# Kernel optimization log

Hardware: AMD Instinct MI355X
Metric: run time of the kernel (lower is better)

## Reference

```python
import jax, jax.numpy as jnp
import numpy as np

NUM_GRAPHS = 4096  # fixed number of segments for scatter_mean


def setup_inputs() -> dict:
    key = jax.random.key(0)
    ks = jax.random.split(key, 8)
    N, D, G = 1_000_000, 256, 256
    s = 1.0 / np.sqrt(D)
    x = jax.random.normal(ks[0], (N, D), dtype=jnp.float32)
    batch = jnp.sort(jax.random.randint(ks[1], (N,), 0, NUM_GRAPHS, dtype=jnp.int64))
    W = jax.random.normal(ks[2], (D, G), dtype=jnp.float32) * s
    b = jax.random.normal(ks[3], (G,), dtype=jnp.float32) * s
    Wg = jax.random.normal(ks[4], (D, G), dtype=jnp.float32) * s
    bg = jax.random.normal(ks[5], (G,), dtype=jnp.float32) * s
    Wf = jax.random.normal(ks[6], (G, G), dtype=jnp.float32) * (1.0 / np.sqrt(G))
    bf = jax.random.normal(ks[7], (G,), dtype=jnp.float32) * (1.0 / np.sqrt(G))
    return {"x": x, "batch": batch, "W": W, "b": b, "Wg": Wg, "bg": bg, "Wf": Wf, "bf": bf}


def reference(x, batch, W, b, Wg, bg, Wf, bf):
    # gated linear: states * softmax(gates) over feature dim (dim=1)
    states = x @ W + b                                   # [N, G]
    gates = jax.nn.softmax(x @ Wg + bg, axis=1)          # [N, G]
    gated = states * gates                               # [N, G]
    # scatter_mean over graph ids
    seg_sum = jax.ops.segment_sum(gated, batch, num_segments=NUM_GRAPHS)
    counts = jax.ops.segment_sum(jnp.ones((x.shape[0],), dtype=gated.dtype), batch,
                                 num_segments=NUM_GRAPHS)
    mean = seg_sum / jnp.maximum(counts, 1.0)[:, None]   # [NUM_GRAPHS, G]
    return mean @ Wf + bf
```

## Files before the change

kernel.cpp:

```cpp
#include <hip/hip_runtime.h>
#include <hip/hip_bf16.h>

typedef __attribute__((ext_vector_type(8))) short short8;
typedef __attribute__((ext_vector_type(4))) float f32x4;

#define D_DIM 256
#define G_DIM 256
#define NSEG 4096
#define BM 64

__device__ __forceinline__ unsigned f2bf_u(float f) {
  unsigned u = __builtin_bit_cast(unsigned, f);
  return (u + 0x7fffu + ((u >> 16) & 1u)) >> 16;
}
__device__ __forceinline__ unsigned pk_bf2(float a, float b) {
  __hip_bfloat162 h = __float22bfloat162_rn(float2{a, b});
  unsigned r;
  __builtin_memcpy(&r, &h, 4);
  return r;
}

__global__ void wconv_kernel(const float* __restrict__ W, const float* __restrict__ Wg,
                             unsigned short* __restrict__ Wc) {
  int j = blockIdx.x;
  int k = threadIdx.x;
  float v = (j < 256) ? W[k * 256 + j] : Wg[k * 256 + (j - 256)];
  Wc[j * 256 + k] = (unsigned short)f2bf_u(v);
}

__global__ void count_kernel(const int* __restrict__ batch, int N, float* __restrict__ counts) {
  int g = blockIdx.x * blockDim.x + threadIdx.x;
  if (g >= NSEG) return;
  int lo = 0, hi = N;
  while (lo < hi) { int mid = (lo + hi) >> 1; if (batch[mid] < g) lo = mid + 1; else hi = mid; }
  int lo2 = lo, hi2 = N;
  while (lo2 < hi2) { int mid = (lo2 + hi2) >> 1; if (batch[mid] < g + 1) lo2 = mid + 1; else hi2 = mid; }
  counts[g] = (float)(lo2 - lo);
}

__global__ __launch_bounds__(512, 4) void fused_main(
    const float* __restrict__ x, const int* __restrict__ batch,
    const unsigned short* __restrict__ Wc,
    const float* __restrict__ bvec, const float* __restrict__ bgvec,
    float* __restrict__ seg, int N) {
  __shared__ __align__(16) char xs[32768];
  __shared__ __align__(16) float part[8][64];
  __shared__ __align__(16) float sinv[64];

  const int t = threadIdx.x;
  const int lane = t & 63;
  const int wid = t >> 6;
  const int lr = lane & 15;
  const int lk = lane >> 4;
  const long row0 = (long)blockIdx.x * BM;

#pragma unroll
  for (int it = 0; it < 4; ++it) {
    int rl = it * 16 + (t >> 5);
    int kb = (t & 31) * 8;
    const float4* p = (const float4*)(x + (row0 + rl) * D_DIM + kb);
    float4 v0 = p[0], v1 = p[1];
    uint4 pk;
    pk.x = pk_bf2(v0.x, v0.y);
    pk.y = pk_bf2(v0.z, v0.w);
    pk.z = pk_bf2(v1.x, v1.y);
    pk.w = pk_bf2(v1.z, v1.w);
    int byte = (rl * 512 + kb * 2) ^ ((rl & 7) << 4);
    *(uint4*)(xs + byte) = pk;
  }
  __syncthreads();

  f32x4 acc[4][4];
#pragma unroll
  for (int m = 0; m < 4; ++m)
#pragma unroll
    for (int n = 0; n < 4; ++n) acc[m][n] = (f32x4){0.f, 0.f, 0.f, 0.f};

  const int cb = wid * 32;
#pragma unroll
  for (int kk = 0; kk < 8; ++kk) {
    const int k0 = kk * 32 + lk * 8;
    short8 a[4], bb[4];
#pragma unroll
    for (int n = 0; n < 4; ++n) {
      int col = (n < 2) ? (cb + n * 16 + lr) : (256 + cb + (n - 2) * 16 + lr);
      bb[n] = *(const short8*)(Wc + col * 256 + k0);
    }
#pragma unroll
    for (int m = 0; m < 4; ++m) {
      int row = m * 16 + lr;
      int byte = (row * 512 + k0 * 2) ^ ((row & 7) << 4);
      a[m] = *(const short8*)(xs + byte);
    }
#pragma unroll
    for (int m = 0; m < 4; ++m)
#pragma unroll
      for (int n = 0; n < 4; ++n)
        acc[m][n] = __builtin_amdgcn_mfma_f32_16x16x32_bf16(a[m], bb[n], acc[m][n], 0, 0, 0);
  }

  float bgv[2];
#pragma unroll
  for (int n = 0; n < 2; ++n) bgv[n] = bgvec[cb + n * 16 + lr];
#pragma unroll
  for (int m = 0; m < 4; ++m)
#pragma unroll
    for (int n = 2; n < 4; ++n)
#pragma unroll
      for (int q = 0; q < 4; ++q)
        acc[m][n][q] = __expf(acc[m][n][q] + bgv[n - 2]);

#pragma unroll
  for (int m = 0; m < 4; ++m) {
    float s[4];
#pragma unroll
    for (int q = 0; q < 4; ++q) {
      float v = acc[m][2][q] + acc[m][3][q];
      v += __shfl_xor(v, 1);
      v += __shfl_xor(v, 2);
      v += __shfl_xor(v, 4);
      v += __shfl_xor(v, 8);
      s[q] = v;
    }
    if (lr == 0) {
#pragma unroll
      for (int q = 0; q < 4; ++q) part[wid][m * 16 + lk * 4 + q] = s[q];
    }
  }
  __syncthreads();
  if (wid == 0) {
    float v = part[0][lane] + part[1][lane] + part[2][lane] + part[3][lane] +
              part[4][lane] + part[5][lane] + part[6][lane] + part[7][lane];
    sinv[lane] = 1.0f / v;
  }
  __syncthreads();

  float bv[2];
#pragma unroll
  for (int n = 0; n < 2; ++n) bv[n] = bvec[cb + n * 16 + lr];
  f32x4 siv[4];
#pragma unroll
  for (int m = 0; m < 4; ++m) siv[m] = *(const f32x4*)(&sinv[m * 16 + lk * 4]);
#pragma unroll
  for (int m = 0; m < 4; ++m)
#pragma unroll
    for (int n = 0; n < 2; ++n)
#pragma unroll
      for (int q = 0; q < 4; ++q)
        acc[m][n][q] = (acc[m][n][q] + bv[n]) * acc[m][n + 2][q] * siv[m][q];

  int rb[4][4];
#pragma unroll
  for (int m = 0; m < 4; ++m) {
    const int4 v = *(const int4*)(batch + row0 + m * 16 + lk * 4);
    rb[m][0] = v.x; rb[m][1] = v.y; rb[m][2] = v.z; rb[m][3] = v.w;
  }
  const int g0 = batch[row0];
  const int g1 = batch[row0 + BM - 1];
  for (int g = g0; g <= g1; ++g) {
    float p[2] = {0.f, 0.f};
#pragma unroll
    for (int m = 0; m < 4; ++m)
#pragma unroll
      for (int q = 0; q < 4; ++q) {
        bool hit = (rb[m][q] == g);
#pragma unroll
        for (int n = 0; n < 2; ++n) p[n] += hit ? acc[m][n][q] : 0.f;
      }
#pragma unroll
    for (int n = 0; n < 2; ++n) {
      p[n] += __shfl_xor(p[n], 16);
      p[n] += __shfl_xor(p[n], 32);
    }
    if (lane < 16) {
#pragma unroll
      for (int n = 0; n < 2; ++n)
        atomicAdd(seg + (long)g * G_DIM + cb + n * 16 + lane, p[n]);
    }
  }
}

__global__ __launch_bounds__(256) void final_kernel(
    float* __restrict__ seg, const float* __restrict__ counts,
    const float* __restrict__ Wf, const float* __restrict__ bfv) {
  __shared__ float mlds[16][257];
  int g0 = blockIdx.x * 16;
  int t = threadIdx.x;
#pragma unroll
  for (int i = 0; i < 16; ++i) {
    float inv = 1.0f / fmaxf(counts[g0 + i], 1.0f);
    mlds[i][t] = seg[(g0 + i) * 256 + t] * inv;
  }
  __syncthreads();
  float a[16];
#pragma unroll
  for (int i = 0; i < 16; ++i) a[i] = 0.f;
  for (int k = 0; k < 256; ++k) {
    float w = Wf[k * 256 + t];
#pragma unroll
    for (int i = 0; i < 16; ++i) a[i] += mlds[i][k] * w;
  }
  float bfx = bfv[t];
#pragma unroll
  for (int i = 0; i < 16; ++i) seg[(g0 + i) * 256 + t] = a[i] + bfx;
}

extern "C" void kernel_launch(void* const* d_in, const int* in_sizes, int n_in,
                              void* d_out, int out_size, void* d_ws, size_t ws_size,
                              hipStream_t stream) {
  const float* x = (const float*)d_in[0];
  const int* batch = (const int*)d_in[1];
  const float* W = (const float*)d_in[2];
  const float* b = (const float*)d_in[3];
  const float* Wg = (const float*)d_in[4];
  const float* bg = (const float*)d_in[5];
  const float* Wf = (const float*)d_in[6];
  const float* bf = (const float*)d_in[7];
  const int N = in_sizes[0] / D_DIM;

  unsigned short* Wc = (unsigned short*)d_ws;
  float* counts = (float*)((char*)d_ws + 262144);
  float* seg = (float*)d_out;

  (void)hipMemsetAsync(d_out, 0, (size_t)out_size * sizeof(float), stream);
  hipLaunchKernelGGL(wconv_kernel, dim3(512), dim3(256), 0, stream, W, Wg, Wc);
  hipLaunchKernelGGL(count_kernel, dim3(NSEG / 256), dim3(256), 0, stream, batch, N, counts);
  hipLaunchKernelGGL(fused_main, dim3(N / BM), dim3(512), 0, stream, x, batch, Wc, b, bg, seg, N);
  hipLaunchKernelGGL(final_kernel, dim3(NSEG / 16), dim3(256), 0, stream, seg, counts, Wf, bf);
}
```

Before: 651.4 us.

## Make fused GEMM kernel persistent with double-buffered LDS and register prefetch

The main kernel becomes persistent: 256 blocks of 1024 threads loop over the 64-row tiles, and each of the 16 waves now owns 16 output columns. The next tile's x rows are prefetched into registers while the current tile is computed, LDS is double-buffered, and B-fragment loads from global memory are software-pipelined two k-steps ahead. The aim is to hide HBM latency for x and cut per-block launch overhead. In exchange, a 1024-thread block carries heavier __syncthreads cost, and 256 blocks may not fill every CU of the device.

After: 935.3 us. +43.6%, slower.

```diff
diff --git a/kernel.cpp b/kernel.cpp
--- a/kernel.cpp
+++ b/kernel.cpp
@@ -8,6 +8,7 @@
 #define G_DIM 256
 #define NSEG 4096
 #define BM 64
+#define PBLK 256
 
 __device__ __forceinline__ unsigned f2bf_u(float f) {
   unsigned u = __builtin_bit_cast(unsigned, f);
@@ -38,13 +39,13 @@
   counts[g] = (float)(lo2 - lo);
 }
 
-__global__ __launch_bounds__(512, 4) void fused_main(
+__global__ __launch_bounds__(1024, 4) void fused_main(
     const float* __restrict__ x, const int* __restrict__ batch,
     const unsigned short* __restrict__ Wc,
     const float* __restrict__ bvec, const float* __restrict__ bgvec,
     float* __restrict__ seg, int N) {
-  __shared__ __align__(16) char xs[32768];
-  __shared__ __align__(16) float part[8][64];
+  __shared__ __align__(16) char xs[2][32768];
+  __shared__ __align__(16) float part[16][64];
   __shared__ __align__(16) float sinv[64];
 
   const int t = threadIdx.x;
@@ -52,130 +53,153 @@
   const int wid = t >> 6;
   const int lr = lane & 15;
   const int lk = lane >> 4;
-  const long row0 = (long)blockIdx.x * BM;
-
-#pragma unroll
-  for (int it = 0; it < 4; ++it) {
-    int rl = it * 16 + (t >> 5);
-    int kb = (t & 31) * 8;
-    const float4* p = (const float4*)(x + (row0 + rl) * D_DIM + kb);
-    float4 v0 = p[0], v1 = p[1];
-    uint4 pk;
-    pk.x = pk_bf2(v0.x, v0.y);
-    pk.y = pk_bf2(v0.z, v0.w);
-    pk.z = pk_bf2(v1.x, v1.y);
-    pk.w = pk_bf2(v1.z, v1.w);
-    int byte = (rl * 512 + kb * 2) ^ ((rl & 7) << 4);
-    *(uint4*)(xs + byte) = pk;
-  }
-  __syncthreads();
-
-  f32x4 acc[4][4];
-#pragma unroll
-  for (int m = 0; m < 4; ++m)
-#pragma unroll
-    for (int n = 0; n < 4; ++n) acc[m][n] = (f32x4){0.f, 0.f, 0.f, 0.f};
-
-  const int cb = wid * 32;
-#pragma unroll
-  for (int kk = 0; kk < 8; ++kk) {
-    const int k0 = kk * 32 + lk * 8;
-    short8 a[4], bb[4];
-#pragma unroll
-    for (int n = 0; n < 4; ++n) {
-      int col = (n < 2) ? (cb + n * 16 + lr) : (256 + cb + (n - 2) * 16 + lr);
-      bb[n] = *(const short8*)(Wc + col * 256 + k0);
-    }
-#pragma unroll
-    for (int m = 0; m < 4; ++m) {
-      int row = m * 16 + lr;
-      int byte = (row * 512 + k0 * 2) ^ ((row & 7) << 4);
-      a[m] = *(const short8*)(xs + byte);
-    }
+  const int cb = wid * 16;
+  const int ntiles = N / BM;
+
+  const int srl = t >> 5;
+  const int skb = (t & 31) * 8;
+  const int sby0 = (srl * 512 + skb * 2) ^ ((srl & 7) << 4);
+  const int sby1 = ((srl + 32) * 512 + skb * 2) ^ (((srl + 32) & 7) << 4);
+
+  const unsigned short* Bs = Wc + (cb + lr) * 256 + lk * 8;
+  const unsigned short* Bg = Wc + (256 + cb + lr) * 256 + lk * 8;
+
+  int abase[4], asw[4];
+#pragma unroll
+  for (int m = 0; m < 4; ++m) {
+    int ar = m * 16 + lr;
+    abase[m] = ar * 512;
+    asw[m] = (ar & 7) << 4;
+  }
+  const int ko2 = lk * 16;
+
+  const float bgv = bgvec[cb + lr];
+  const float bv = bvec[cb + lr];
+
+  int tile = blockIdx.x;
+  float4 ld0, ld1, ld2, ld3;
+  {
+    const float* p0 = x + (long)(tile * BM + srl) * D_DIM + skb;
+    ld0 = ((const float4*)p0)[0];
+    ld1 = ((const float4*)p0)[1];
+    const float* p1 = p0 + 32 * D_DIM;
+    ld2 = ((const float4*)p1)[0];
+    ld3 = ((const float4*)p1)[1];
+  }
+
+  for (int it = 0; tile < ntiles; ++it, tile += PBLK) {
+    char* xb = xs[it & 1];
+    const long row0 = (long)tile * BM;
+
+    {
+      uint4 pk0, pk1;
+      pk0.x = pk_bf2(ld0.x, ld0.y); pk0.y = pk_bf2(ld0.z, ld0.w);
+      pk0.z = pk_bf2(ld1.x, ld1.y); pk0.w = pk_bf2(ld1.z, ld1.w);
+      pk1.x = pk_bf2(ld2.x, ld2.y); pk1.y = pk_bf2(ld2.z, ld2.w);
+      pk1.z = pk_bf2(ld3.x, ld3.y); pk1.w = pk_bf2(ld3.z, ld3.w);
+      *(uint4*)(xb + sby0) = pk0;
+      *(uint4*)(xb + sby1) = pk1;
+    }
+    if (tile + PBLK < ntiles) {
+      const float* p0 = x + ((long)(tile + PBLK) * BM + srl) * D_DIM + skb;
+      ld0 = ((const float4*)p0)[0];
+      ld1 = ((const float4*)p0)[1];
+      const float* p1 = p0 + 32 * D_DIM;
+      ld2 = ((const float4*)p1)[0];
+      ld3 = ((const float4*)p1)[1];
+    }
+
+    short8 bcur0 = *(const short8*)(Bs);
+    short8 bcur1 = *(const short8*)(Bg);
+    short8 bnxt0 = *(const short8*)(Bs + 32);
+    short8 bnxt1 = *(const short8*)(Bg + 32);
+
+    __syncthreads();
+
+    f32x4 acc[4][2];
+#pragma unroll
+    for (int m = 0; m < 4; ++m) {
+      acc[m][0] = (f32x4){0.f, 0.f, 0.f, 0.f};
+      acc[m][1] = (f32x4){0.f, 0.f, 0.f, 0.f};
+    }
+
+#pragma unroll
+    for (int kk = 0; kk < 8; ++kk) {
+      short8 a[4];
+#pragma unroll
+      for (int m = 0; m < 4; ++m)
+        a[m] = *(const short8*)(xb + abase[m] + ((kk * 64 + ko2) ^ asw[m]));
+      short8 b0 = bcur0, b1 = bcur1;
+      bcur0 = bnxt0; bcur1 = bnxt1;
+      if (kk < 6) {
+        bnxt0 = *(const short8*)(Bs + (kk + 2) * 32);
+        bnxt1 = *(const short8*)(Bg + (kk + 2) * 32);
+      }
+#pragma unroll
+      for (int m = 0; m < 4; ++m) {
+        acc[m][0] = __builtin_amdgcn_mfma_f32_16x16x32_bf16(a[m], b0, acc[m][0], 0, 0, 0);
+        acc[m][1] = __builtin_amdgcn_mfma_f32_16x16x32_bf16(a[m], b1, acc[m][1], 0, 0, 0);
+      }
+    }
+
 #pragma unroll
     for (int m = 0; m < 4; ++m)
 #pragma unroll
-      for (int n = 0; n < 4; ++n)
-        acc[m][n] = __builtin_amdgcn_mfma_f32_16x16x32_bf16(a[m], bb[n], acc[m][n], 0, 0, 0);
-  }
-
-  float bgv[2];
-#pragma unroll
-  for (int n = 0; n < 2; ++n) bgv[n] = bgvec[cb + n * 16 + lr];
-#pragma unroll
-  for (int m = 0; m < 4; ++m)
-#pragma unroll
-    for (int n = 2; n < 4; ++n)
-#pragma unroll
       for (int q = 0; q < 4; ++q)
-        acc[m][n][q] = __expf(acc[m][n][q] + bgv[n - 2]);
-
-#pragma unroll
-  for (int m = 0; m < 4; ++m) {
-    float s[4];
-#pragma unroll
-    for (int q = 0; q < 4; ++q) {
-      float v = acc[m][2][q] + acc[m][3][q];
-      v += __shfl_xor(v, 1);
-      v += __shfl_xor(v, 2);
-      v += __shfl_xor(v, 4);
-      v += __shfl_xor(v, 8);
-      s[q] = v;
-    }
-    if (lr == 0) {
-#pragma unroll
-      for (int q = 0; q < 4; ++q) part[wid][m * 16 + lk * 4 + q] = s[q];
-    }
-  }
-  __syncthreads();
-  if (wid == 0) {
-    float v = part[0][lane] + part[1][lane] + part[2][lane] + part[3][lane] +
-              part[4][lane] + part[5][lane] + part[6][lane] + part[7][lane];
-    sinv[lane] = 1.0f / v;
-  }
-  __syncthreads();
-
-  float bv[2];
-#pragma unroll
-  for (int n = 0; n < 2; ++n) bv[n] = bvec[cb + n * 16 + lr];
-  f32x4 siv[4];
-#pragma unroll
-  for (int m = 0; m < 4; ++m) siv[m] = *(const f32x4*)(&sinv[m * 16 + lk * 4]);
-#pragma unroll
-  for (int m = 0; m < 4; ++m)
-#pragma unroll
-    for (int n = 0; n < 2; ++n)
+        acc[m][1][q] = __expf(acc[m][1][q] + bgv);
+
+#pragma unroll
+    for (int m = 0; m < 4; ++m) {
+      float s[4];
+#pragma unroll
+      for (int q = 0; q < 4; ++q) {
+        float v = acc[m][1][q];
+        v += __shfl_xor(v, 1);
+        v += __shfl_xor(v, 2);
+        v += __shfl_xor(v, 4);
+        v += __shfl_xor(v, 8);
+        s[q] = v;
+      }
+      if (lr == 0) {
+#pragma unroll
+        for (int q = 0; q < 4; ++q) part[wid][m * 16 + lk * 4 + q] = s[q];
+      }
+    }
+    __syncthreads();
+    if (wid == 0) {
+      float v = 0.f;
+#pragma unroll
+      for (int w = 0; w < 16; ++w) v += part[w][lane];
+      sinv[lane] = 1.0f / v;
+    }
+    __syncthreads();
+
+#pragma unroll
+    for (int m = 0; m < 4; ++m) {
+      f32x4 siv = *(const f32x4*)(&sinv[m * 16 + lk * 4]);
 #pragma unroll
       for (int q = 0; q < 4; ++q)
-        acc[m][n][q] = (acc[m][n][q] + bv[n]) * acc[m][n + 2][q] * siv[m][q];
-
-  int rb[4][4];
-#pragma unroll
-  for (int m = 0; m < 4; ++m) {
-    const int4 v = *(const int4*)(batch + row0 + m * 16 + lk * 4);
-    rb[m][0] = v.x; rb[m][1] = v.y; rb[m][2] = v.z; rb[m][3] = v.w;
-  }
-  const int g0 = batch[row0];
-  const int g1 = batch[row0 + BM - 1];
-  for (int g = g0; g <= g1; ++g) {
-    float p[2] = {0.f, 0.f};
-#pragma unroll
-    for (int m = 0; m < 4; ++m)
-#pragma unroll
-      for (int q = 0; q < 4; ++q) {
-        bool hit = (rb[m][q] == g);
-#pragma unroll
-        for (int n = 0; n < 2; ++n) p[n] += hit ? acc[m][n][q] : 0.f;
-      }
-#pragma unroll
-    for (int n = 0; n < 2; ++n) {
-      p[n] += __shfl_xor(p[n], 16);
-      p[n] += __shfl_xor(p[n], 32);
-    }
-    if (lane < 16) {
-#pragma unroll
-      for (int n = 0; n < 2; ++n)
-        atomicAdd(seg + (long)g * G_DIM + cb + n * 16 + lane, p[n]);
+        acc[m][0][q] = (acc[m][0][q] + bv) * acc[m][1][q] * siv[q];
+    }
+
+    int rb[4][4];
+#pragma unroll
+    for (int m = 0; m < 4; ++m) {
+      const int4 v = *(const int4*)(batch + row0 + m * 16 + lk * 4);
+      rb[m][0] = v.x; rb[m][1] = v.y; rb[m][2] = v.z; rb[m][3] = v.w;
+    }
+    const int g0 = batch[row0];
+    const int g1 = batch[row0 + BM - 1];
+    for (int g = g0; g <= g1; ++g) {
+      float p = 0.f;
+#pragma unroll
+      for (int m = 0; m < 4; ++m)
+#pragma unroll
+        for (int q = 0; q < 4; ++q)
+          p += (rb[m][q] == g) ? acc[m][0][q] : 0.f;
+      p += __shfl_xor(p, 16);
+      p += __shfl_xor(p, 32);
+      if (lane < 16) atomicAdd(seg + (long)g * G_DIM + cb + lane, p);
     }
   }
 }
@@ -225,6 +249,6 @@
   (void)hipMemsetAsync(d_out, 0, (size_t)out_size * sizeof(float), stream);
   hipLaunchKernelGGL(wconv_kernel, dim3(512), dim3(256), 0, stream, W, Wg, Wc);
   hipLaunchKernelGGL(count_kernel, dim3(NSEG / 256), dim3(256), 0, stream, batch, N, counts);
-  hipLaunchKernelGGL(fused_main, dim3(N / BM), dim3(512), 0, stream, x, batch, Wc, b, bg, seg, N);
+  hipLaunchKernelGGL(fused_main, dim3(PBLK), dim3(1024), 0, stream, x, batch, Wc, b, bg, seg, N);
   hipLaunchKernelGGL(final_kernel, dim3(NSEG / 16), dim3(256), 0, stream, seg, counts, Wf, bf);
 }
```

## Make fused kernel persistent with double-buffered x tiles and carried segment accumulation

Applied to the files above, without the earlier changes.

The fused GEMM/softmax/scatter kernel becomes persistent: 256 blocks each walk a contiguous range of 64-row tiles. The next tile's x is prefetched into registers and staged into a second LDS buffer while the current tile is computed. B-operand loads are software-pipelined across k steps. Segment partial sums are carried across tiles, so atomics are issued only when the graph id changes, which cuts atomic traffic. The cost is that only 256 blocks (occupancy hint 2) must saturate HBM bandwidth, leaving less latency hiding than many small blocks would give.

Result: slower. 861.2 us (+32.2%).

```diff
diff --git a/kernel.cpp b/kernel.cpp
--- a/kernel.cpp
+++ b/kernel.cpp
@@ -8,6 +8,7 @@
 #define G_DIM 256
 #define NSEG 4096
 #define BM 64
+#define PBLK 256
 
 __device__ __forceinline__ unsigned f2bf_u(float f) {
   unsigned u = __builtin_bit_cast(unsigned, f);
@@ -38,12 +39,12 @@
   counts[g] = (float)(lo2 - lo);
 }
 
-__global__ __launch_bounds__(512, 4) void fused_main(
+__global__ __launch_bounds__(512, 2) void fused_main(
     const float* __restrict__ x, const int* __restrict__ batch,
     const unsigned short* __restrict__ Wc,
     const float* __restrict__ bvec, const float* __restrict__ bgvec,
     float* __restrict__ seg, int N) {
-  __shared__ __align__(16) char xs[32768];
+  __shared__ __align__(16) char xs[2][32768];
   __shared__ __align__(16) float part[8][64];
   __shared__ __align__(16) float sinv[64];
 
@@ -52,132 +53,208 @@
   const int wid = t >> 6;
   const int lr = lane & 15;
   const int lk = lane >> 4;
-  const long row0 = (long)blockIdx.x * BM;
-
+  const int cb = wid * 32;
+  const int ntiles = N / BM;
+
+  const int q = ntiles / PBLK, r = ntiles % PBLK;
+  const int bid = blockIdx.x;
+  const int t0 = bid * q + (bid < r ? bid : r);
+  const int t1 = t0 + q + (bid < r ? 1 : 0);
+
+  const int srl = t >> 5;
+  const int skb = (t & 31) * 8;
+  int sby[4];
 #pragma unroll
   for (int it = 0; it < 4; ++it) {
-    int rl = it * 16 + (t >> 5);
-    int kb = (t & 31) * 8;
-    const float4* p = (const float4*)(x + (row0 + rl) * D_DIM + kb);
-    float4 v0 = p[0], v1 = p[1];
-    uint4 pk;
-    pk.x = pk_bf2(v0.x, v0.y);
-    pk.y = pk_bf2(v0.z, v0.w);
-    pk.z = pk_bf2(v1.x, v1.y);
-    pk.w = pk_bf2(v1.z, v1.w);
-    int byte = (rl * 512 + kb * 2) ^ ((rl & 7) << 4);
-    *(uint4*)(xs + byte) = pk;
-  }
+    int rl = it * 16 + srl;
+    sby[it] = (rl * 512 + skb * 2) ^ ((rl & 7) << 4);
+  }
+
+  const unsigned short* Bp[4];
+#pragma unroll
+  for (int n = 0; n < 4; ++n) {
+    int col = (n < 2) ? (cb + n * 16 + lr) : (256 + cb + (n - 2) * 16 + lr);
+    Bp[n] = Wc + col * 256 + lk * 8;
+  }
+
+  int abase[4], asw[4];
+#pragma unroll
+  for (int m = 0; m < 4; ++m) {
+    int ar = m * 16 + lr;
+    abase[m] = ar * 512;
+    asw[m] = (ar & 7) << 4;
+  }
+  const int ko2 = lk * 16;
+
+  float bgv[2], bv[2];
+#pragma unroll
+  for (int n = 0; n < 2; ++n) {
+    bgv[n] = bgvec[cb + n * 16 + lr];
+    bv[n] = bvec[cb + n * 16 + lr];
+  }
+
+  float4 L[4][2];
+#define LOADX(tt)                                                     \
+  {                                                                   \
+    const float* p_ = x + ((long)(tt)*BM + srl) * D_DIM + skb;        \
+    _Pragma("unroll") for (int i_ = 0; i_ < 4; ++i_) {                \
+      L[i_][0] = ((const float4*)p_)[0];                              \
+      L[i_][1] = ((const float4*)p_)[1];                              \
+      p_ += 16 * D_DIM;                                               \
+    }                                                                 \
+  }
+#define STAGEX(xb_)                                                   \
+  {                                                                   \
+    _Pragma("unroll") for (int i_ = 0; i_ < 4; ++i_) {                \
+      uint4 pk_;                                                      \
+      pk_.x = pk_bf2(L[i_][0].x, L[i_][0].y);                         \
+      pk_.y = pk_bf2(L[i_][0].z, L[i_][0].w);                         \
+      pk_.z = pk_bf2(L[i_][1].x, L[i_][1].y);                         \
+      pk_.w = pk_bf2(L[i_][1].z, L[i_][1].w);                         \
+      *(uint4*)((xb_) + sby[i_]) = pk_;                               \
+    }                                                                 \
+  }
+
+  LOADX(t0);
+  STAGEX(xs[0]);
+  if (t0 + 1 < t1) LOADX(t0 + 1);
   __syncthreads();
 
-  f32x4 acc[4][4];
-#pragma unroll
-  for (int m = 0; m < 4; ++m)
-#pragma unroll
-    for (int n = 0; n < 4; ++n) acc[m][n] = (f32x4){0.f, 0.f, 0.f, 0.f};
-
-  const int cb = wid * 32;
-#pragma unroll
-  for (int kk = 0; kk < 8; ++kk) {
-    const int k0 = kk * 32 + lk * 8;
-    short8 a[4], bb[4];
+  int gcur = batch[(long)t0 * BM];
+  float pacc[2] = {0.f, 0.f};
+
+  for (int tt = t0; tt < t1; ++tt) {
+    const int it = tt - t0;
+    char* xb = xs[it & 1];
+    const long row0 = (long)tt * BM;
+
+    short8 bcur[4], bnxt[4];
 #pragma unroll
     for (int n = 0; n < 4; ++n) {
-      int col = (n < 2) ? (cb + n * 16 + lr) : (256 + cb + (n - 2) * 16 + lr);
-      bb[n] = *(const short8*)(Wc + col * 256 + k0);
-    }
+      bcur[n] = *(const short8*)(Bp[n]);
+      bnxt[n] = *(const short8*)(Bp[n] + 32);
+    }
+
+    f32x4 acc[4][4];
+#pragma unroll
+    for (int m = 0; m < 4; ++m)
+#pragma unroll
+      for (int n = 0; n < 4; ++n) acc[m][n] = (f32x4){0.f, 0.f, 0.f, 0.f};
+
+#pragma unroll
+    for (int kk = 0; kk < 8; ++kk) {
+      short8 a[4];
+#pragma unroll
+      for (int m = 0; m < 4; ++m)
+        a[m] = *(const short8*)(xb + abase[m] + ((kk * 64 + ko2) ^ asw[m]));
+      short8 b0[4];
+#pragma unroll
+      for (int n = 0; n < 4; ++n) {
+        b0[n] = bcur[n];
+        bcur[n] = bnxt[n];
+      }
+      if (kk < 6) {
+#pragma unroll
+        for (int n = 0; n < 4; ++n) bnxt[n] = *(const short8*)(Bp[n] + (kk + 2) * 32);
+      }
+#pragma unroll
+      for (int m = 0; m < 4; ++m)
+#pragma unroll
+        for (int n = 0; n < 4; ++n)
+          acc[m][n] = __builtin_amdgcn_mfma_f32_16x16x32_bf16(a[m], b0[n], acc[m][n], 0, 0, 0);
+    }
+
+#pragma unroll
+    for (int m = 0; m < 4; ++m)
+#pragma unroll
+      for (int n = 2; n < 4; ++n)
+#pragma unroll
+        for (int qq = 0; qq < 4; ++qq)
+          acc[m][n][qq] = __expf(acc[m][n][qq] + bgv[n - 2]);
+
 #pragma unroll
     for (int m = 0; m < 4; ++m) {
-      int row = m * 16 + lr;
-      int byte = (row * 512 + k0 * 2) ^ ((row & 7) << 4);
-      a[m] = *(const short8*)(xs + byte);
-    }
-#pragma unroll
-    for (int m = 0; m < 4; ++m)
-#pragma unroll
-      for (int n = 0; n < 4; ++n)
-        acc[m][n] = __builtin_amdgcn_mfma_f32_16x16x32_bf16(a[m], bb[n], acc[m][n], 0, 0, 0);
-  }
-
-  float bgv[2];
-#pragma unroll
-  for (int n = 0; n < 2; ++n) bgv[n] = bgvec[cb + n * 16 + lr];
-#pragma unroll
-  for (int m = 0; m < 4; ++m)
-#pragma unroll
-    for (int n = 2; n < 4; ++n)
-#pragma unroll
-      for (int q = 0; q < 4; ++q)
-        acc[m][n][q] = __expf(acc[m][n][q] + bgv[n - 2]);
-
-#pragma unroll
-  for (int m = 0; m < 4; ++m) {
-    float s[4];
-#pragma unroll
-    for (int q = 0; q < 4; ++q) {
-      float v = acc[m][2][q] + acc[m][3][q];
-      v += __shfl_xor(v, 1);
-      v += __shfl_xor(v, 2);
-      v += __shfl_xor(v, 4);
-      v += __shfl_xor(v, 8);
-      s[q] = v;
-    }
-    if (lr == 0) {
-#pragma unroll
-      for (int q = 0; q < 4; ++q) part[wid][m * 16 + lk * 4 + q] = s[q];
-    }
-  }
-  __syncthreads();
-  if (wid == 0) {
-    float v = part[0][lane] + part[1][lane] + part[2][lane] + part[3][lane] +
-              part[4][lane] + part[5][lane] + part[6][lane] + part[7][lane];
-    sinv[lane] = 1.0f / v;
-  }
-  __syncthreads();
-
-  float bv[2];
-#pragma unroll
-  for (int n = 0; n < 2; ++n) bv[n] = bvec[cb + n * 16 + lr];
-  f32x4 siv[4];
-#pragma unroll
-  for (int m = 0; m < 4; ++m) siv[m] = *(const f32x4*)(&sinv[m * 16 + lk * 4]);
-#pragma unroll
-  for (int m = 0; m < 4; ++m)
-#pragma unroll
-    for (int n = 0; n < 2; ++n)
-#pragma unroll
-      for (int q = 0; q < 4; ++q)
-        acc[m][n][q] = (acc[m][n][q] + bv[n]) * acc[m][n + 2][q] * siv[m][q];
-
-  int rb[4][4];
-#pragma unroll
-  for (int m = 0; m < 4; ++m) {
-    const int4 v = *(const int4*)(batch + row0 + m * 16 + lk * 4);
-    rb[m][0] = v.x; rb[m][1] = v.y; rb[m][2] = v.z; rb[m][3] = v.w;
-  }
-  const int g0 = batch[row0];
-  const int g1 = batch[row0 + BM - 1];
-  for (int g = g0; g <= g1; ++g) {
-    float p[2] = {0.f, 0.f};
-#pragma unroll
-    for (int m = 0; m < 4; ++m)
-#pragma unroll
-      for (int q = 0; q < 4; ++q) {
-        bool hit = (rb[m][q] == g);
-#pragma unroll
-        for (int n = 0; n < 2; ++n) p[n] += hit ? acc[m][n][q] : 0.f;
-      }
-#pragma unroll
-    for (int n = 0; n < 2; ++n) {
-      p[n] += __shfl_xor(p[n], 16);
-      p[n] += __shfl_xor(p[n], 32);
-    }
+      float s[4];
+#pragma unroll
+      for (int qq = 0; qq < 4; ++qq) {
+        float v = acc[m][2][qq] + acc[m][3][qq];
+        v += __shfl_xor(v, 1);
+        v += __shfl_xor(v, 2);
+        v += __shfl_xor(v, 4);
+        v += __shfl_xor(v, 8);
+        s[qq] = v;
+      }
+      if (lr == 0) {
+#pragma unroll
+        for (int qq = 0; qq < 4; ++qq) part[wid][m * 16 + lk * 4 + qq] = s[qq];
+      }
+    }
+    __syncthreads();
+    if (wid == 0) {
+      float v = part[0][lane] + part[1][lane] + part[2][lane] + part[3][lane] +
+                part[4][lane] + part[5][lane] + part[6][lane] + part[7][lane];
+      sinv[lane] = 1.0f / v;
+    }
+    __syncthreads();
+
+#pragma unroll
+    for (int m = 0; m < 4; ++m) {
+      f32x4 siv = *(const f32x4*)(&sinv[m * 16 + lk * 4]);
+#pragma unroll
+      for (int n = 0; n < 2; ++n)
+#pragma unroll
+        for (int qq = 0; qq < 4; ++qq)
+          acc[m][n][qq] = (acc[m][n][qq] + bv[n]) * acc[m][n + 2][qq] * siv[qq];
+    }
+
+    int rb[4][4];
+#pragma unroll
+    for (int m = 0; m < 4; ++m) {
+      const int4 v = *(const int4*)(batch + row0 + m * 16 + lk * 4);
+      rb[m][0] = v.x; rb[m][1] = v.y; rb[m][2] = v.z; rb[m][3] = v.w;
+    }
+    const int g0 = batch[row0];
+    const int g1 = batch[row0 + BM - 1];
+    for (int g = g0; g <= g1; ++g) {
+      if (g != gcur) {
+        float p0 = pacc[0], p1 = pacc[1];
+        p0 += __shfl_xor(p0, 16); p0 += __shfl_xor(p0, 32);
+        p1 += __shfl_xor(p1, 16); p1 += __shfl_xor(p1, 32);
+        if (lane < 16) {
+          atomicAdd(seg + (long)gcur * G_DIM + cb + lane, p0);
+          atomicAdd(seg + (long)gcur * G_DIM + cb + 16 + lane, p1);
+        }
+        pacc[0] = 0.f; pacc[1] = 0.f;
+        gcur = g;
+      }
+#pragma unroll
+      for (int m = 0; m < 4; ++m)
+#pragma unroll
+        for (int qq = 0; qq < 4; ++qq) {
+          bool hit = (rb[m][qq] == g);
+          pacc[0] += hit ? acc[m][0][qq] : 0.f;
+          pacc[1] += hit ? acc[m][1][qq] : 0.f;
+        }
+    }
+
+    if (tt + 1 < t1) {
+      STAGEX(xs[(it + 1) & 1]);
+      if (tt + 2 < t1) LOADX(tt + 2);
+    }
+    __syncthreads();
+  }
+
+  {
+    float p0 = pacc[0], p1 = pacc[1];
+    p0 += __shfl_xor(p0, 16); p0 += __shfl_xor(p0, 32);
+    p1 += __shfl_xor(p1, 16); p1 += __shfl_xor(p1, 32);
     if (lane < 16) {
-#pragma unroll
-      for (int n = 0; n < 2; ++n)
-        atomicAdd(seg + (long)g * G_DIM + cb + n * 16 + lane, p[n]);
-    }
-  }
+      atomicAdd(seg + (long)gcur * G_DIM + cb + lane, p0);
+      atomicAdd(seg + (long)gcur * G_DIM + cb + 16 + lane, p1);
+    }
+  }
+#undef LOADX
+#undef STAGEX
 }
 
 __global__ __launch_bounds__(256) void final_kernel(
@@ -225,6 +302,6 @@
   (void)hipMemsetAsync(d_out, 0, (size_t)out_size * sizeof(float), stream);
   hipLaunchKernelGGL(wconv_kernel, dim3(512), dim3(256), 0, stream, W, Wg, Wc);
   hipLaunchKernelGGL(count_kernel, dim3(NSEG / 256), dim3(256), 0, stream, batch, N, counts);
-  hipLaunchKernelGGL(fused_main, dim3(N / BM), dim3(512), 0, stream, x, batch, Wc, b, bg, seg, N);
+  hipLaunchKernelGGL(fused_main, dim3(PBLK), dim3(512), 0, stream, x, batch, Wc, b, bg, seg, N);
   hipLaunchKernelGGL(final_kernel, dim3(NSEG / 16), dim3(256), 0, stream, seg, counts, Wf, bf);
 }
```
